# Kernel tuning notes

Measured on AMD Instinct MI355X. Metric: run time of the kernel, lower is better.

Reference implementation:

```python
import jax, jax.numpy as jnp
import numpy as np

B, L, H, NH = 2, 2048, 1024, 16
HD = H // NH  # head dim = 64


def setup_inputs() -> dict:
    key = jax.random.key(0)
    ks = jax.random.split(key, 8)
    s = 0.02  # small init scale for weights
    return {
        "q": jax.random.normal(ks[0], (B, L, H), jnp.float32),
        "k": jax.random.normal(ks[1], (B, L, H), jnp.float32),
        "v": jax.random.normal(ks[2], (B, L, H), jnp.float32),
        "attention_mask": jnp.zeros((B, NH, L, L), jnp.float32),
        "Wq": jax.random.normal(ks[3], (H, H), jnp.float32) * s,
        "bq": jnp.zeros((H,), jnp.float32),
        "Wk": jax.random.normal(ks[4], (H, H), jnp.float32) * s,
        "bk": jnp.zeros((H,), jnp.float32),
        "Wv": jax.random.normal(ks[5], (H, H), jnp.float32) * s,
        "bv": jnp.zeros((H,), jnp.float32),
        "Wo": jax.random.normal(ks[6], (H, H), jnp.float32) * s,
        "bo": jnp.zeros((H,), jnp.float32),
    }


def reference(q, k, v, attention_mask, Wq, bq, Wk, bk, Wv, bv, Wo, bo):
    # Conv1D (GPT-2 style) projections: x @ W + b
    query = q @ Wq + bq  # [B, L, H]
    key = k @ Wk + bk
    value = v @ Wv + bv
    # split heads -> [B, NH, L, HD]
    qh = query.reshape(B, L, NH, HD).transpose(0, 2, 1, 3)
    kh = key.reshape(B, L, NH, HD).transpose(0, 2, 1, 3)
    vh = value.reshape(B, L, NH, HD).transpose(0, 2, 1, 3)
    # scores: [B, NH, L, L]
    w = jnp.einsum("bhqd,bhkd->bhqk", qh, kh) / jnp.sqrt(jnp.float32(HD))
    w = w + attention_mask
    w = jax.nn.softmax(w, axis=-1)  # dropout p=0 -> identity
    out = jnp.einsum("bhqk,bhkd->bhqd", w, vh)  # [B, NH, L, HD]
    # merge heads -> [B, L, H]
    out = out.transpose(0, 2, 1, 3).reshape(B, L, H)
    return out @ Wo + bo
```

## Files before the change

kernel.cpp:

```cpp
#include <hip/hip_runtime.h>

#define NBATCH 2
#define LSEQ   2048
#define NH     16
#define HD     64
#define HDIM   1024
#define MTOK   4096

typedef unsigned short u16;
typedef __attribute__((ext_vector_type(8))) short bf16x8;
typedef __attribute__((ext_vector_type(4))) float f32x4;

__device__ __forceinline__ u16 f2bf(float f) {
  union { float f; unsigned int u; } x; x.f = f;
  return (u16)((x.u + 0x7fffu + ((x.u >> 16) & 1u)) >> 16);
}

__device__ __forceinline__ void gload_lds16(const void* g, void* l) {
  __builtin_amdgcn_global_load_lds(
      (const __attribute__((address_space(1))) unsigned int*)g,
      (__attribute__((address_space(3))) unsigned int*)l, 16, 0, 0);
}

__global__ void prep_kernel(
    const float* __restrict__ q, const float* __restrict__ k, const float* __restrict__ v,
    const float* __restrict__ W0, const float* __restrict__ W1,
    const float* __restrict__ W2, const float* __restrict__ W3,
    u16* __restrict__ xq, u16* __restrict__ xk, u16* __restrict__ xv,
    u16* __restrict__ T0, u16* __restrict__ T1, u16* __restrict__ T2,
    u16* __restrict__ T3) {
  __shared__ float tile[64][65];
  if (blockIdx.z < 3) {
    const float* in = (blockIdx.z == 0) ? q : (blockIdx.z == 1) ? k : v;
    u16* out = (blockIdx.z == 0) ? xq : (blockIdx.z == 1) ? xk : xv;
    int i = blockIdx.x * blockDim.x + threadIdx.x;
    float4 t4 = ((const float4*)in)[i];
    ushort4 o;
    o.x = f2bf(t4.x); o.y = f2bf(t4.y); o.z = f2bf(t4.z); o.w = f2bf(t4.w);
    ((ushort4*)out)[i] = o;
    return;
  }
  if (blockIdx.x >= 1024) return;
  const int sel = blockIdx.x >> 8, bx = blockIdx.x & 255;
  const float* W = (sel == 0) ? W0 : (sel == 1) ? W1 : (sel == 2) ? W2 : W3;
  u16* Wt = (sel == 0) ? T0 : (sel == 1) ? T1 : (sel == 2) ? T2 : T3;
  const int k0 = (bx & 15) << 6;
  const int n0 = (bx >> 4) << 6;
  const int t = threadIdx.x;
#pragma unroll
  for (int i = 0; i < 4; ++i) {
    int idx = t + i * 256;
    int r = idx >> 4, c = (idx & 15) << 2;
    float4 v4 = *(const float4*)&W[(size_t)(k0 + r) * HDIM + n0 + c];
    tile[r][c] = v4.x; tile[r][c + 1] = v4.y; tile[r][c + 2] = v4.z; tile[r][c + 3] = v4.w;
  }
  __syncthreads();
#pragma unroll
  for (int i = 0; i < 4; ++i) {
    int idx = t + i * 256;
    int r = idx >> 4, c = (idx & 15) << 2;
    ushort4 o;
    o.x = f2bf(tile[c][r]);     o.y = f2bf(tile[c + 1][r]);
    o.z = f2bf(tile[c + 2][r]); o.w = f2bf(tile[c + 3][r]);
    *(ushort4*)&Wt[(size_t)(n0 + r) * HDIM + k0 + c] = o;
  }
}

template <int MODE>
__device__ __forceinline__ void gemm_core(u16* As, u16* Bs, int m0, int n0,
    const u16* __restrict__ A, const u16* __restrict__ Bt,
    const float* __restrict__ bias, void* __restrict__ Cout) {
  const int tid = threadIdx.x;
  const int lane = tid & 63, wid = tid >> 6;
  const int l15 = lane & 15, g = lane >> 4;
  const int wr = wid >> 1, wc = wid & 1;
  f32x4 acc[4][4];
#pragma unroll
  for (int i = 0; i < 4; ++i)
#pragma unroll
    for (int j = 0; j < 4; ++j) acc[i][j] = (f32x4){0.f, 0.f, 0.f, 0.f};

  for (int t = 0; t < HDIM / 64; ++t) {
    const int k0 = t * 64;
    __syncthreads();
#pragma unroll
    for (int i = 0; i < 4; ++i) {
      const int row = wid * 32 + i * 8 + (lane >> 3);
      const int colb = (lane & 7) * 16;
      gload_lds16((const char*)(A + (size_t)(m0 + row) * HDIM + k0) + colb,
                  (char*)As + (wid * 32 + i * 8) * 128);
      gload_lds16((const char*)(Bt + (size_t)(n0 + row) * HDIM + k0) + colb,
                  (char*)Bs + (wid * 32 + i * 8) * 128);
    }
    __syncthreads();
#pragma unroll
    for (int ks = 0; ks < 2; ++ks) {
      bf16x8 a[4], b[4];
#pragma unroll
      for (int i = 0; i < 4; ++i) {
        const int row = wr * 64 + i * 16 + l15;
        a[i] = *(const bf16x8*)((const char*)As + row * 128 + ks * 64 + g * 16);
      }
#pragma unroll
      for (int j = 0; j < 4; ++j) {
        const int row = wc * 64 + j * 16 + l15;
        b[j] = *(const bf16x8*)((const char*)Bs + row * 128 + ks * 64 + g * 16);
      }
#pragma unroll
      for (int i = 0; i < 4; ++i)
#pragma unroll
        for (int j = 0; j < 4; ++j)
          acc[i][j] = __builtin_amdgcn_mfma_f32_16x16x32_bf16(a[i], b[j], acc[i][j], 0, 0, 0);
    }
  }
#pragma unroll
  for (int i = 0; i < 4; ++i) {
    const int mrow = m0 + wr * 64 + i * 16 + 4 * g;
#pragma unroll
    for (int j = 0; j < 4; ++j) {
      const int ncol = n0 + wc * 64 + j * 16 + l15;
      const float bb = bias[ncol];
      if (MODE == 2) {
        const int bidx = mrow >> 11, l0 = mrow & (LSEQ - 1);
        const int h = ncol >> 6, d = ncol & 63;
        ushort4 o4;
        o4.x = f2bf(acc[i][j][0] + bb); o4.y = f2bf(acc[i][j][1] + bb);
        o4.z = f2bf(acc[i][j][2] + bb); o4.w = f2bf(acc[i][j][3] + bb);
        *(ushort4*)&((u16*)Cout)[(((size_t)bidx * NH + h) * HD + d) * LSEQ + l0] = o4;
      } else {
        const int h = ncol >> 6, d = ncol & 63;
        u16* o = (u16*)Cout;
#pragma unroll
        for (int r = 0; r < 4; ++r) {
          const int m = mrow + r;
          const int bidx = m >> 11, l = m & (LSEQ - 1);
          o[(((size_t)bidx * NH + h) * LSEQ + l) * HD + d] = f2bf(acc[i][j][r] + bb);
        }
      }
    }
  }
}

__global__ __launch_bounds__(256, 3) void proj_gemm_kernel(
    const u16* __restrict__ xq, const u16* __restrict__ xk, const u16* __restrict__ xv,
    const u16* __restrict__ WqT, const u16* __restrict__ WkT, const u16* __restrict__ WvT,
    const float* __restrict__ bq, const float* __restrict__ bk, const float* __restrict__ bv,
    u16* __restrict__ Qh, u16* __restrict__ Kh, u16* __restrict__ Vt) {
  __shared__ u16 As[128 * 64];
  __shared__ u16 Bs[128 * 64];
  const int h = blockIdx.x;
  const int l = (h & 7) * 96 + (h >> 3);
  const int z = l >> 8, rem = l & 255;
  const int m0 = (rem >> 3) * 128, n0 = (rem & 7) * 128;
  if (z == 0)      gemm_core<0>(As, Bs, m0, n0, xq, WqT, bq, Qh);
  else if (z == 1) gemm_core<0>(As, Bs, m0, n0, xk, WkT, bk, Kh);
  else             gemm_core<2>(As, Bs, m0, n0, xv, WvT, bv, Vt);
}

__global__ __launch_bounds__(256, 3) void out_gemm_kernel(
    const u16* __restrict__ A, const u16* __restrict__ WoT,
    const float* __restrict__ bo, float* __restrict__ out) {
  __shared__ u16 As[64 * 64];
  __shared__ u16 Bs[128 * 64];
  const int h = blockIdx.x;
  const int l = (h & 7) * 64 + (h >> 3);
  const int m0 = (l >> 3) * 64, n0 = (l & 7) * 128;
  const int lane = threadIdx.x & 63, w = threadIdx.x >> 6;
  const int l15 = lane & 15, g = lane >> 4;
  f32x4 acc[8];
#pragma unroll
  for (int j = 0; j < 8; ++j) acc[j] = (f32x4){0.f, 0.f, 0.f, 0.f};

  for (int t = 0; t < HDIM / 64; ++t) {
    const int k0 = t * 64;
    __syncthreads();
    const int colb = (lane & 7) * 16;
#pragma unroll
    for (int i = 0; i < 2; ++i) {
      const int row = w * 16 + i * 8 + (lane >> 3);
      gload_lds16((const char*)(A + (size_t)(m0 + row) * HDIM + k0) + colb,
                  (char*)As + (w * 16 + i * 8) * 128);
    }
#pragma unroll
    for (int i = 0; i < 4; ++i) {
      const int row = w * 32 + i * 8 + (lane >> 3);
      gload_lds16((const char*)(WoT + (size_t)(n0 + row) * HDIM + k0) + colb,
                  (char*)Bs + (w * 32 + i * 8) * 128);
    }
    __syncthreads();
#pragma unroll
    for (int ks = 0; ks < 2; ++ks) {
      bf16x8 a = *(const bf16x8*)((const char*)As + (w * 16 + l15) * 128 + ks * 64 + g * 16);
#pragma unroll
      for (int j = 0; j < 8; ++j) {
        bf16x8 b = *(const bf16x8*)((const char*)Bs + (j * 16 + l15) * 128 + ks * 64 + g * 16);
        acc[j] = __builtin_amdgcn_mfma_f32_16x16x32_bf16(a, b, acc[j], 0, 0, 0);
      }
    }
  }
#pragma unroll
  for (int j = 0; j < 8; ++j) {
    const int ncol = n0 + j * 16 + l15;
    const float bb = bo[ncol];
#pragma unroll
    for (int r = 0; r < 4; ++r)
      out[(size_t)(m0 + w * 16 + 4 * g + r) * HDIM + ncol] = acc[j][r] + bb;
  }
}

__global__ __launch_bounds__(512, 4) void attn_kernel(
    const u16* __restrict__ Qh, const u16* __restrict__ Kh,
    const u16* __restrict__ Vt, const float* __restrict__ mask,
    u16* __restrict__ Out ) {
  __shared__ u16 Ks[2][64 * 64];
  __shared__ u16 Vs[2][64 * 64];
  __shared__ u16 Ps[8][16 * 64];
  const int lane = threadIdx.x & 63, w = threadIdx.x >> 6;
  const int l15 = lane & 15, g = lane >> 4;
  const int kk = blockIdx.x >> 3, xcd = blockIdx.x & 7;
  const int bh = xcd * 4 + (kk >> 4);
  const int qb = kk & 15;
  const int q0 = qb * 128 + w * 16;
  const int NT = LSEQ / 64;

  bf16x8 aq[2];
  {
    const u16* qbase = Qh + ((size_t)bh * LSEQ + q0 + l15) * HD;
    aq[0] = *(const bf16x8*)(qbase + g * 8);
    aq[1] = *(const bf16x8*)(qbase + 32 + g * 8);
  }
  f32x4 o_acc[4];
#pragma unroll
  for (int db = 0; db < 4; ++db) o_acc[db] = (f32x4){0.f, 0.f, 0.f, 0.f};
  float m_run = -1e30f, l_run = 0.f;

  const size_t kbase = (size_t)bh * LSEQ * HD;
  const size_t vbase = (size_t)bh * HD * LSEQ;
  const int srow = w * 8 + (lane >> 3);
  const int scolb = (lane & 7) * 16;

#define STAGE(buf, tt) do {                                                    \
    const int kv0_ = (tt) * 64;                                                \
    const int cb_ = scolb ^ ((srow & 7) << 4);                                 \
    gload_lds16((const char*)(Kh + kbase + (size_t)(kv0_ + srow) * HD) + cb_,  \
                (char*)Ks[buf] + (w * 8) * 128);                               \
    gload_lds16((const char*)(Vt + vbase + (size_t)srow * LSEQ + kv0_) + cb_,  \
                (char*)Vs[buf] + (w * 8) * 128);                               \
  } while (0)

  const float* mrow = mask + ((size_t)bh * LSEQ + q0 + l15) * LSEQ;
  f32x4 mvA[4], mvB[4];

  STAGE(0, 0);
#pragma unroll
  for (int mb = 0; mb < 4; ++mb) {
    mvA[mb] = __builtin_nontemporal_load((const f32x4*)(mrow + 0 * 64 + mb * 16 + 4 * g));
    mvB[mb] = __builtin_nontemporal_load((const f32x4*)(mrow + 1 * 64 + mb * 16 + 4 * g));
  }
  __syncthreads();

  u16* pbase = Ps[w];
  const int srcbase = (lane & 48) | ((lane & 48) >> 2);
  const int pswz = (l15 & 7) << 4;

#define TILE_BODY(t, cur, mv) do {                                            \
    if ((t) + 1 < NT) STAGE((cur) ^ 1, (t) + 1);                              \
               \
    f32x4 s_acc[4];                                                           \
    _Pragma("unroll")                                                         \
    for (int mb = 0; mb < 4; ++mb) s_acc[mb] = (f32x4){0.f, 0.f, 0.f, 0.f};   \
    __builtin_amdgcn_s_setprio(1);                                            \
    _Pragma("unroll")                                                         \
    for (int ks = 0; ks < 2; ++ks) {                                          \
      _Pragma("unroll")                                                       \
      for (int mb = 0; mb < 4; ++mb) {                                        \
        const int row = mb * 16 + l15;                                        \
        bf16x8 bk = *(const bf16x8*)((const char*)Ks[cur] + row * 128 +       \
                                     ((ks * 64 + g * 16) ^ ((row & 7) << 4)));\
        s_acc[mb] = __builtin_amdgcn_mfma_f32_16x16x32_bf16(bk, aq[ks],       \
                                                            s_acc[mb], 0,0,0);\
      }                                                                       \
    }                                                                         \
    __builtin_amdgcn_s_setprio(0);                                            \
                              \
    float p[4][4];                                                            \
    float tmax = -1e30f;                                                      \
    _Pragma("unroll")                                                         \
    for (int mb = 0; mb < 4; ++mb)                                            \
      _Pragma("unroll")                                                       \
      for (int r = 0; r < 4; ++r) {                                           \
        p[mb][r] = s_acc[mb][r] * 0.125f + mv[mb][r];                         \
        tmax = fmaxf(tmax, p[mb][r]);                                         \
      }                                                                       \
    tmax = fmaxf(tmax, __shfl_xor(tmax, 16));                                 \
    tmax = fmaxf(tmax, __shfl_xor(tmax, 32));                                 \
    if (!__all(tmax - m_run <= 8.f)) {                     \
      const float mnew = fmaxf(m_run, tmax);                                  \
      const float cf = __expf(m_run - mnew);                                  \
      m_run = mnew;                                                           \
      l_run *= cf;                                                            \
      float cfr[4];                                                           \
      _Pragma("unroll")                                                       \
      for (int r = 0; r < 4; ++r) cfr[r] = __shfl(cf, srcbase + r);           \
      _Pragma("unroll")                                                       \
      for (int db = 0; db < 4; ++db)                                          \
        _Pragma("unroll")                                                     \
        for (int r = 0; r < 4; ++r) o_acc[db][r] *= cfr[r];                   \
    }                                                                         \
    float psum = 0.f;                                                         \
    _Pragma("unroll")                                                         \
    for (int mb = 0; mb < 4; ++mb)                                            \
      _Pragma("unroll")                                                       \
      for (int r = 0; r < 4; ++r) {                                           \
        p[mb][r] = __expf(p[mb][r] - m_run);                                  \
        psum += p[mb][r];                                                     \
      }                                                                       \
    psum += __shfl_xor(psum, 16);                                             \
    psum += __shfl_xor(psum, 32);                                             \
    l_run += psum;                                                            \
                             \
    _Pragma("unroll")                                                         \
    for (int mb = 0; mb < 4; ++mb) {                                          \
      ushort4 pk;                                                             \
      pk.x = f2bf(p[mb][0]); pk.y = f2bf(p[mb][1]);                           \
      pk.z = f2bf(p[mb][2]); pk.w = f2bf(p[mb][3]);                           \
      *(ushort4*)((char*)pbase + l15 * 128 + ((mb * 32 + 8 * g) ^ pswz)) = pk;\
    }                                                                         \
                    \
    __builtin_amdgcn_sched_barrier(0);                                        \
    {                                                                         \
      const int tn = ((t) + 2 < NT) ? (t) + 2 : NT - 1;                       \
      const float* mnext = mrow + tn * 64;                                    \
      _Pragma("unroll")                                                       \
      for (int mb = 0; mb < 4; ++mb)                                          \
        mv[mb] = __builtin_nontemporal_load(                                  \
            (const f32x4*)(mnext + mb * 16 + 4 * g));                         \
    }                                                                         \
                      \
    asm volatile("s_waitcnt lgkmcnt(0)" ::: "memory");                        \
    __builtin_amdgcn_sched_barrier(0);                                        \
                                                                \
    __builtin_amdgcn_s_setprio(1);                                            \
    _Pragma("unroll")                                                         \
    for (int s = 0; s < 2; ++s) {                                             \
      bf16x8 pa = *(const bf16x8*)((const char*)pbase + l15 * 128 +           \
                                   ((s * 64 + 16 * g) ^ pswz));               \
      _Pragma("unroll")                                                       \
      for (int db = 0; db < 4; ++db) {                                        \
        const int row = db * 16 + l15;                                        \
        bf16x8 bv = *(const bf16x8*)((const char*)Vs[cur] + row * 128 +       \
                                     ((s * 64 + 16 * g) ^ ((row & 7) << 4))); \
        o_acc[db] = __builtin_amdgcn_mfma_f32_16x16x32_bf16(pa, bv,           \
                                                            o_acc[db], 0,0,0);\
      }                                                                       \
    }                                                                         \
    __builtin_amdgcn_s_setprio(0);                                            \
    \
    asm volatile("s_waitcnt vmcnt(4)" ::: "memory");                          \
    __builtin_amdgcn_s_barrier();                                             \
    __builtin_amdgcn_sched_barrier(0);                                        \
  } while (0)

  for (int t = 0; t < NT; t += 2) {
    TILE_BODY(t, 0, mvA);
    TILE_BODY(t + 1, 1, mvB);
  }
#undef TILE_BODY
#undef STAGE

  const int b = bh >> 4, h = bh & 15;
  float lr[4];
#pragma unroll
  for (int r = 0; r < 4; ++r) lr[r] = __shfl(l_run, srcbase + r);
#pragma unroll
  for (int r = 0; r < 4; ++r) {
    const float inv = 1.f / lr[r];
    const int qg = q0 + 4 * g + r;
    u16* orow = Out + ((size_t)(b * LSEQ + qg) * NH + h) * HD;
#pragma unroll
    for (int db = 0; db < 4; ++db)
      orow[db * 16 + l15] = f2bf(o_acc[db][r] * inv);
  }
}

extern "C" void kernel_launch(void* const* d_in, const int* in_sizes, int n_in,
                              void* d_out, int out_size, void* d_ws, size_t ws_size,
                              hipStream_t stream) {
  (void)in_sizes; (void)n_in; (void)out_size; (void)ws_size;
  const float* q    = (const float*)d_in[0];
  const float* k    = (const float*)d_in[1];
  const float* v    = (const float*)d_in[2];
  const float* mask = (const float*)d_in[3];
  const float* Wq   = (const float*)d_in[4];
  const float* bq   = (const float*)d_in[5];
  const float* Wk   = (const float*)d_in[6];
  const float* bk   = (const float*)d_in[7];
  const float* Wv   = (const float*)d_in[8];
  const float* bv   = (const float*)d_in[9];
  const float* Wo   = (const float*)d_in[10];
  const float* bo   = (const float*)d_in[11];
  float* out = (float*)d_out;

  char* ws = (char*)d_ws;
  const size_t XB = (size_t)MTOK * HDIM * 2;
  const size_t WB = (size_t)HDIM * HDIM * 2;
  u16* xq   = (u16*)(ws);
  u16* xk   = (u16*)(ws + XB);
  u16* xv   = (u16*)(ws + 2 * XB);
  u16* WqT  = (u16*)(ws + 3 * XB);
  u16* WkT  = (u16*)(ws + 3 * XB + WB);
  u16* WvT  = (u16*)(ws + 3 * XB + 2 * WB);
  u16* WoT  = (u16*)(ws + 3 * XB + 3 * WB);
  u16* Qh   = (u16*)(ws + 3 * XB + 4 * WB);
  u16* Kh   = (u16*)(ws + 4 * XB + 4 * WB);
  u16* Vt   = (u16*)(ws + 5 * XB + 4 * WB);
  u16* aout = (u16*)(ws + 6 * XB + 4 * WB);

  prep_kernel<<<dim3((MTOK * HDIM) / 4 / 256, 1, 4), 256, 0, stream>>>(
      q, k, v, Wq, Wk, Wv, Wo, xq, xk, xv, WqT, WkT, WvT, WoT);
  proj_gemm_kernel<<<768, 256, 0, stream>>>(
      xq, xk, xv, WqT, WkT, WvT, bq, bk, bv, Qh, Kh, Vt);
  attn_kernel<<<512, 512, 0, stream>>>(Qh, Kh, Vt, mask, aout);
  out_gemm_kernel<<<512, 256, 0, stream>>>(aout, WoT, bo, out);
}
```

Before: 226.1 us.

## Retile output GEMM to 128x64 with 2x2 warp grid; use plain mask loads

The output projection GEMM moves from a 64x128 block tile with 1x8 MFMA per warp to a 128x64 tile where the four warps form a 2x2 grid, each computing 4x2 MFMA subtiles. This reuses each A and B fragment read from LDS across more MFMAs, cutting LDS reads per MFMA, and launch bounds drop to 2 blocks per SM. The attention kernel's mask loads change from nontemporal loads to ordinary cached loads, which could help or hurt depending on cache behaviour.

```diff
diff --git a/kernel.cpp b/kernel.cpp
--- a/kernel.cpp
+++ b/kernel.cpp
@@ -157,54 +157,71 @@
   else             gemm_core<2>(As, Bs, m0, n0, xv, WvT, bv, Vt);
 }
 
-__global__ __launch_bounds__(256, 3) void out_gemm_kernel(
+__global__ __launch_bounds__(256, 2) void out_gemm_kernel(
     const u16* __restrict__ A, const u16* __restrict__ WoT,
     const float* __restrict__ bo, float* __restrict__ out) {
-  __shared__ u16 As[64 * 64];
-  __shared__ u16 Bs[128 * 64];
+  __shared__ u16 As[128 * 64];
+  __shared__ u16 Bs[64 * 64];
   const int h = blockIdx.x;
   const int l = (h & 7) * 64 + (h >> 3);
-  const int m0 = (l >> 3) * 64, n0 = (l & 7) * 128;
-  const int lane = threadIdx.x & 63, w = threadIdx.x >> 6;
+  const int m0 = (l >> 4) * 128, n0 = (l & 15) * 64;
+  const int lane = threadIdx.x & 63, wid = threadIdx.x >> 6;
   const int l15 = lane & 15, g = lane >> 4;
-  f32x4 acc[8];
-#pragma unroll
-  for (int j = 0; j < 8; ++j) acc[j] = (f32x4){0.f, 0.f, 0.f, 0.f};
+  const int wr = wid >> 1, wc = wid & 1;
+  f32x4 acc[4][2];
+#pragma unroll
+  for (int i = 0; i < 4; ++i)
+#pragma unroll
+    for (int j = 0; j < 2; ++j) acc[i][j] = (f32x4){0.f, 0.f, 0.f, 0.f};
 
   for (int t = 0; t < HDIM / 64; ++t) {
     const int k0 = t * 64;
     __syncthreads();
     const int colb = (lane & 7) * 16;
 #pragma unroll
+    for (int i = 0; i < 4; ++i) {
+      const int row = wid * 32 + i * 8 + (lane >> 3);
+      gload_lds16((const char*)(A + (size_t)(m0 + row) * HDIM + k0) + colb,
+                  (char*)As + (wid * 32 + i * 8) * 128);
+    }
+#pragma unroll
     for (int i = 0; i < 2; ++i) {
-      const int row = w * 16 + i * 8 + (lane >> 3);
-      gload_lds16((const char*)(A + (size_t)(m0 + row) * HDIM + k0) + colb,
-                  (char*)As + (w * 16 + i * 8) * 128);
-    }
-#pragma unroll
-    for (int i = 0; i < 4; ++i) {
-      const int row = w * 32 + i * 8 + (lane >> 3);
+      const int row = wid * 16 + i * 8 + (lane >> 3);
       gload_lds16((const char*)(WoT + (size_t)(n0 + row) * HDIM + k0) + colb,
-                  (char*)Bs + (w * 32 + i * 8) * 128);
+                  (char*)Bs + (wid * 16 + i * 8) * 128);
     }
     __syncthreads();
 #pragma unroll
     for (int ks = 0; ks < 2; ++ks) {
-      bf16x8 a = *(const bf16x8*)((const char*)As + (w * 16 + l15) * 128 + ks * 64 + g * 16);
-#pragma unroll
-      for (int j = 0; j < 8; ++j) {
-        bf16x8 b = *(const bf16x8*)((const char*)Bs + (j * 16 + l15) * 128 + ks * 64 + g * 16);
-        acc[j] = __builtin_amdgcn_mfma_f32_16x16x32_bf16(a, b, acc[j], 0, 0, 0);
+      bf16x8 a[4], b[2];
+#pragma unroll
+      for (int i = 0; i < 4; ++i) {
+        const int row = wr * 64 + i * 16 + l15;
+        a[i] = *(const bf16x8*)((const char*)As + row * 128 + ks * 64 + g * 16);
       }
-    }
-  }
-#pragma unroll
-  for (int j = 0; j < 8; ++j) {
-    const int ncol = n0 + j * 16 + l15;
-    const float bb = bo[ncol];
-#pragma unroll
-    for (int r = 0; r < 4; ++r)
-      out[(size_t)(m0 + w * 16 + 4 * g + r) * HDIM + ncol] = acc[j][r] + bb;
+#pragma unroll
+      for (int j = 0; j < 2; ++j) {
+        const int row = wc * 32 + j * 16 + l15;
+        b[j] = *(const bf16x8*)((const char*)Bs + row * 128 + ks * 64 + g * 16);
+      }
+#pragma unroll
+      for (int i = 0; i < 4; ++i)
+#pragma unroll
+        for (int j = 0; j < 2; ++j)
+          acc[i][j] = __builtin_amdgcn_mfma_f32_16x16x32_bf16(a[i], b[j], acc[i][j], 0, 0, 0);
+    }
+  }
+#pragma unroll
+  for (int i = 0; i < 4; ++i) {
+    const int mrow = m0 + wr * 64 + i * 16 + 4 * g;
+#pragma unroll
+    for (int j = 0; j < 2; ++j) {
+      const int ncol = n0 + wc * 32 + j * 16 + l15;
+      const float bb = bo[ncol];
+#pragma unroll
+      for (int r = 0; r < 4; ++r)
+        out[(size_t)(mrow + r) * HDIM + ncol] = acc[i][j][r] + bb;
+    }
   }
 }
 
@@ -254,8 +271,8 @@
   STAGE(0, 0);
 #pragma unroll
   for (int mb = 0; mb < 4; ++mb) {
-    mvA[mb] = __builtin_nontemporal_load((const f32x4*)(mrow + 0 * 64 + mb * 16 + 4 * g));
-    mvB[mb] = __builtin_nontemporal_load((const f32x4*)(mrow + 1 * 64 + mb * 16 + 4 * g));
+    mvA[mb] = *(const f32x4*)(mrow + 0 * 64 + mb * 16 + 4 * g);
+    mvB[mb] = *(const f32x4*)(mrow + 1 * 64 + mb * 16 + 4 * g);
   }
   __syncthreads();
 
@@ -326,15 +343,14 @@
       pk.z = f2bf(p[mb][2]); pk.w = f2bf(p[mb][3]);                           \
       *(ushort4*)((char*)pbase + l15 * 128 + ((mb * 32 + 8 * g) ^ pswz)) = pk;\
     }                                                                         \
-                    \
+           \
     __builtin_amdgcn_sched_barrier(0);                                        \
     {                                                                         \
       const int tn = ((t) + 2 < NT) ? (t) + 2 : NT - 1;                       \
       const float* mnext = mrow + tn * 64;                                    \
       _Pragma("unroll")                                                       \
       for (int mb = 0; mb < 4; ++mb)                                          \
-        mv[mb] = __builtin_nontemporal_load(                                  \
-            (const f32x4*)(mnext + mb * 16 + 4 * g));                         \
+        mv[mb] = *(const f32x4*)(mnext + mb * 16 + 4 * g);                    \
     }                                                                         \
                       \
     asm volatile("s_waitcnt lgkmcnt(0)" ::: "memory");                        \
```

New measurement: 215.8 us. 4.5% less time.
